# Kernel tuning notes

Hardware: AMD Instinct MI355X
Metric: run time of the kernel (lower is better)

Reference implementation:

```python
import jax, jax.numpy as jnp
import numpy as np

B, N, H, T = 4096, 512, 1024, 10  # batch, input_size, hidden_size, num_iterations
NUM_OPS = 20


def setup_inputs() -> dict:
    key = jax.random.key(0)
    k1, k2, k3, k4 = jax.random.split(key, 4)
    return {
        "x": jax.random.normal(k1, (B, N, 1), jnp.float32),
        "frozen_weight": jax.random.normal(k2, (1, N, H), jnp.float32) / np.sqrt(H),
        "alpha": jax.random.normal(k3, (T, NUM_OPS), jnp.float32),
        "layer_beta": jax.random.normal(k4, (T, 2), jnp.float32),
    }


def _softshrink(x, lam):
    return jnp.where(x > lam, x - lam, jnp.where(x < -lam, x + lam, jnp.zeros_like(x)))


def _hardshrink(x, lam):
    return jnp.where(jnp.abs(x) > lam, x, jnp.zeros_like(x))


def _make_ops(lam):
    # Same 20 ops, same order as the torch ModuleList.
    return [
        lambda x: _softshrink(x, lam),                 # Softshrink(0.001/L)
        jax.nn.relu,                                   # ReLU
        lambda x: x,                                   # Identity
        lambda x: jax.nn.gelu(x, approximate=False),   # GELU (exact erf, torch default)
        jax.nn.elu,                                    # ELU
        lambda x: _hardshrink(x, lam),                 # Hardshrink(0.001/L)
        lambda x: jnp.clip(x, -1.0, 1.0),              # Hardtanh
        jax.nn.hard_swish,                             # Hardswish
        jax.nn.selu,                                   # SELU
        jax.nn.celu,                                   # CELU
        jax.nn.leaky_relu,                             # LeakyReLU (slope 0.01)
        jax.nn.log_sigmoid,                            # LogSigmoid
        lambda x: x - jnp.tanh(x),                     # Tanhshrink
        jax.nn.soft_sign,                              # Softsign
        jax.nn.softplus,                               # Softplus
        jnp.tanh,                                      # Tanh
        jax.nn.sigmoid,                                # Sigmoid
        jax.nn.hard_sigmoid,                           # Hardsigmoid
        jax.nn.silu,                                   # SiLU
        lambda x: x * jnp.tanh(jax.nn.softplus(x)),    # Mish
    ]


def _forward(x, frozen_weight, alpha, layer_beta):
    W = frozen_weight[0]                       # [N, H]
    L = jnp.linalg.norm(W, ord=2) ** 2         # spectral norm squared (Lipschitz)
    lam = 0.001 / L
    ops = _make_ops(lam)

    b = x.shape[0]
    hidden = W.shape[1]
    z = jnp.zeros((b, hidden, 1), dtype=x.dtype)
    z_prev = z
    num_iters = alpha.shape[0]
    for i in range(num_iters):
        aw = jax.nn.softmax(alpha[i])          # [20] (training path, eval_flag=False)
        bw = jax.nn.softmax(layer_beta[i])     # [2]
        # FISTA-style momentum + frozen-weight gradient step
        z_aux = z + (i / (i + 3)) * (z - z_prev)      # [B,H,1]
        Wz = jnp.einsum('nh,bho->bno', W, z_aux)      # [B,N,1]
        grad = jnp.einsum('nh,bno->bho', W, Wz - x)   # [B,H,1]
        z_g = z_aux - grad / L
        # 20-way weighted activation mixture
        z_op = aw[0] * ops[0](z_g)
        for w, op in zip(aw[1:], ops[1:]):
            z_op = z_op + w * op(z_g)
        # beta-weighted residual mix becomes z_prev; z_op becomes current_z
        z_prev = z * bw[0] + z_op * bw[1]
        z = z_op
    return z


def reference(x, frozen_weight, alpha, layer_beta):
    return _forward(x, frozen_weight, alpha, layer_beta)
```

## Files before the change

kernel.cpp:

```cpp
#include <hip/hip_runtime.h>
#include <hip/hip_bf16.h>

#define DI __device__ __forceinline__

typedef float f32x4 __attribute__((ext_vector_type(4)));
typedef __bf16 bf16x8 __attribute__((ext_vector_type(8)));
using bf16_t = __hip_bfloat16;
using ushort_t = unsigned short;

DI void gload_lds16(const void* g, void* l) {
  __builtin_amdgcn_global_load_lds(
      (const __attribute__((address_space(1))) void*)g,
      (__attribute__((address_space(3))) void*)l, 16, 0, 0);
}

DI float rcpf(float x) { return __builtin_amdgcn_rcpf(x); }

DI float act_mix(float x, const float* aw, float lam) {
  const float ax  = fabsf(x);
  const float en  = __expf(-ax);
  const float en2 = en * en;
  const float i1  = rcpf(1.0f + en);
  const float sig = (x >= 0.0f) ? i1 : en * i1;
  const float th  = copysignf((1.0f - en2) * rcpf(1.0f + en2), x);
  const float l1p = __logf(1.0f + en);
  const float sp  = fmaxf(x, 0.0f) + l1p;
  const float lsg = fminf(x, 0.0f) - l1p;
  const float q   = ((x >= 0.0f) ? en2 : 1.0f) * (i1 * i1);
  const float mish = x * (1.0f - q) * rcpf(1.0f + q);
  const float u  = 0.7071067811865476f * x;
  const float au = fabsf(u);
  const float t  = rcpf(1.0f + 0.3275911f * au);
  float poly = fmaf(t, 1.061405429f, -1.453152027f);
  poly = fmaf(t, poly, 1.421413741f);
  poly = fmaf(t, poly, -0.284496736f);
  poly = fmaf(t, poly, 0.254829592f);
  poly *= t;
  const float erfa = 1.0f - poly * __expf(-u * u);
  const float gelu = 0.5f * x * (1.0f + copysignf(erfa, x));
  const float em1  = en - 1.0f;
  const float elu  = (x > 0.0f) ? x : em1;
  const float selu = (x > 0.0f) ? 1.0507009873554805f * x : 1.7580993408473766f * em1;
  const float relu = fmaxf(x, 0.0f);
  const float t6   = fminf(fmaxf(x + 3.0f, 0.0f), 6.0f) * 0.16666666666666666f;
  const float ssh  = (x > lam) ? (x - lam) : ((x < -lam) ? (x + lam) : 0.0f);
  const float hsh  = (ax > lam) ? x : 0.0f;
  const float htan = fminf(fmaxf(x, -1.0f), 1.0f);
  const float lky  = (x >= 0.0f) ? x : 0.01f * x;
  const float ssn  = x * rcpf(1.0f + ax);
  float r = aw[0] * ssh;
  r = fmaf(aw[1],  relu,   r);
  r = fmaf(aw[2],  x,      r);
  r = fmaf(aw[3],  gelu,   r);
  r = fmaf(aw[4],  elu,    r);
  r = fmaf(aw[5],  hsh,    r);
  r = fmaf(aw[6],  htan,   r);
  r = fmaf(aw[7],  x * t6, r);
  r = fmaf(aw[8],  selu,   r);
  r = fmaf(aw[9],  elu,    r);
  r = fmaf(aw[10], lky,    r);
  r = fmaf(aw[11], lsg,    r);
  r = fmaf(aw[12], x - th, r);
  r = fmaf(aw[13], ssn,    r);
  r = fmaf(aw[14], sp,     r);
  r = fmaf(aw[15], th,     r);
  r = fmaf(aw[16], sig,    r);
  r = fmaf(aw[17], t6,     r);
  r = fmaf(aw[18], x * sig, r);
  r = fmaf(aw[19], mish,   r);
  return r;
}

__global__ void k_prep(const float* __restrict__ W, const float* __restrict__ x,
                       bf16_t* __restrict__ Whi, bf16_t* __restrict__ Wlo,
                       bf16_t* __restrict__ Wth, bf16_t* __restrict__ Wtl,
                       bf16_t* __restrict__ xh, bf16_t* __restrict__ xl) {
  int i = blockIdx.x * 256 + threadIdx.x;
  if (i < 512 * 1024) {
    float w = W[i];
    bf16_t h = __float2bfloat16(w);
    bf16_t l = __float2bfloat16(w - __bfloat162float(h));
    Whi[i] = h; Wlo[i] = l;
    int n = i >> 10, hc = i & 1023;
    Wth[hc * 512 + n] = h; Wtl[hc * 512 + n] = l;
  }
  int j = i - 512 * 1024;
  if (j >= 0 && j < 4096 * 512) {
    float v = x[j];
    bf16_t h = __float2bfloat16(v);
    xh[j] = h;
    xl[j] = __float2bfloat16(v - __bfloat162float(h));
  }
}

template <int KDIM, bool FIRST, bool WF32>
__global__ __launch_bounds__(256) void k_sqm(
    const bf16_t* __restrict__ Xhi, const bf16_t* __restrict__ Xlo,
    bf16_t* __restrict__ Chi, bf16_t* __restrict__ Clo,
    float* __restrict__ Cf,
    const float* __restrict__ pin, float* __restrict__ pout) {
  __shared__ __align__(16) ushort_t Ah[2][32 * 64], Al[2][32 * 64],
                                    Bh[2][32 * 64], Bl[2][32 * 64];
  __shared__ float red[4];
  const int tid = threadIdx.x, lane = tid & 63, wave = tid >> 6;
  const int wm = wave >> 1, wn = wave & 1;
  const int i0 = blockIdx.x * 32, j0 = blockIdx.y * 32;
  const int bid = blockIdx.y * gridDim.x + blockIdx.x;
  const int r16 = lane & 15, kg = lane >> 4;

  float s = 1.0f;
  if constexpr (!FIRST) {
    float v = pin[tid];
    for (int off = 32; off; off >>= 1) v += __shfl_down(v, off, 64);
    if ((tid & 63) == 0) red[tid >> 6] = v;
    __syncthreads();
    s = 1.0f / (red[0] + red[1] + red[2] + red[3]);
    __syncthreads();
  }

  const int row = tid >> 3;
  const int srcc = (((tid & 7) ^ (row & 7)) << 3);
  const long abase = (long)(i0 + row) * KDIM + srcc;
  const long bbase = (long)(j0 + row) * KDIM + srcc;
  const int ldst = tid * 8;

  auto stage = [&](int buf, int kt) {
    gload_lds16(Xhi + abase + kt, &Ah[buf][ldst]);
    gload_lds16(Xlo + abase + kt, &Al[buf][ldst]);
    gload_lds16(Xhi + bbase + kt, &Bh[buf][ldst]);
    gload_lds16(Xlo + bbase + kt, &Bl[buf][ldst]);
  };

  f32x4 acc = {};
  constexpr int NT = KDIM / 64;
  stage(0, 0);
  __syncthreads();
  for (int t = 0; t < NT; ++t) {
    if (t + 1 < NT) stage((t + 1) & 1, (t + 1) * 64);
    const int b = t & 1;
    const int ra = wm * 16 + r16, rb = wn * 16 + r16;
#pragma unroll
    for (int kk = 0; kk < 64; kk += 32) {
      int oa = ra * 64 + ((kk + kg * 8) ^ ((ra & 7) * 8));
      int ob = rb * 64 + ((kk + kg * 8) ^ ((rb & 7) * 8));
      bf16x8 ah = *(const bf16x8*)&Ah[b][oa];
      bf16x8 al = *(const bf16x8*)&Al[b][oa];
      bf16x8 bh = *(const bf16x8*)&Bh[b][ob];
      bf16x8 bl = *(const bf16x8*)&Bl[b][ob];
      acc = __builtin_amdgcn_mfma_f32_16x16x32_bf16(ah, bh, acc, 0, 0, 0);
      acc = __builtin_amdgcn_mfma_f32_16x16x32_bf16(ah, bl, acc, 0, 0, 0);
      acc = __builtin_amdgcn_mfma_f32_16x16x32_bf16(al, bh, acc, 0, 0, 0);
    }
    __syncthreads();
  }

  float fro = 0.0f;
#pragma unroll
  for (int r = 0; r < 4; ++r) {
    float c = acc[r] * s;
    int orow = i0 + wm * 16 + (lane >> 4) * 4 + r;
    int ocol = j0 + wn * 16 + r16;
    int idx = orow * 512 + ocol;
    bf16_t h = __float2bfloat16(c);
    Chi[idx] = h;
    Clo[idx] = __float2bfloat16(c - __bfloat162float(h));
    if constexpr (WF32) Cf[idx] = c;
    fro = fmaf(c, c, fro);
  }
  for (int off = 32; off; off >>= 1) fro += __shfl_down(fro, off, 64);
  if ((tid & 63) == 0) red[tid >> 6] = fro;
  __syncthreads();
  if (tid == 0) pout[bid] = red[0] + red[1] + red[2] + red[3];
}

__global__ __launch_bounds__(256) void k_G(const bf16_t* __restrict__ Xhi,
                                           const bf16_t* __restrict__ Xlo,
                                           bf16_t* __restrict__ G) {
  __shared__ __align__(16) ushort_t Ah[2][32 * 64], Al[2][32 * 64],
                                    Bh[2][32 * 64], Bl[2][32 * 64];
  const int tid = threadIdx.x, lane = tid & 63, wave = tid >> 6;
  const int wm = wave >> 1, wn = wave & 1;
  const int i0 = blockIdx.x * 32, j0 = blockIdx.y * 32;
  const int r16 = lane & 15, kg = lane >> 4;
  const int row = tid >> 3;
  const int srcc = (((tid & 7) ^ (row & 7)) << 3);
  const long abase = (long)(i0 + row) * 512 + srcc;
  const long bbase = (long)(j0 + row) * 512 + srcc;
  const int ldst = tid * 8;

  auto stage = [&](int buf, int kt) {
    gload_lds16(Xhi + abase + kt, &Ah[buf][ldst]);
    gload_lds16(Xlo + abase + kt, &Al[buf][ldst]);
    gload_lds16(Xhi + bbase + kt, &Bh[buf][ldst]);
    gload_lds16(Xlo + bbase + kt, &Bl[buf][ldst]);
  };

  f32x4 acc = {};
  stage(0, 0);
  __syncthreads();
  for (int t = 0; t < 8; ++t) {
    if (t + 1 < 8) stage((t + 1) & 1, (t + 1) * 64);
    const int b = t & 1;
    const int ra = wm * 16 + r16, rb = wn * 16 + r16;
#pragma unroll
    for (int kk = 0; kk < 64; kk += 32) {
      int oa = ra * 64 + ((kk + kg * 8) ^ ((ra & 7) * 8));
      int ob = rb * 64 + ((kk + kg * 8) ^ ((rb & 7) * 8));
      bf16x8 ah = *(const bf16x8*)&Ah[b][oa];
      bf16x8 al = *(const bf16x8*)&Al[b][oa];
      bf16x8 bh = *(const bf16x8*)&Bh[b][ob];
      bf16x8 bl = *(const bf16x8*)&Bl[b][ob];
      acc = __builtin_amdgcn_mfma_f32_16x16x32_bf16(ah, bh, acc, 0, 0, 0);
      acc = __builtin_amdgcn_mfma_f32_16x16x32_bf16(ah, bl, acc, 0, 0, 0);
      acc = __builtin_amdgcn_mfma_f32_16x16x32_bf16(al, bh, acc, 0, 0, 0);
    }
    __syncthreads();
  }
#pragma unroll
  for (int r = 0; r < 4; ++r) {
    int orow = i0 + wm * 16 + (lane >> 4) * 4 + r;
    int ocol = j0 + wn * 16 + r16;
    G[orow * 1024 + ocol] = __float2bfloat16(acc[r]);
  }
}

__global__ __launch_bounds__(256) void k_xw(const bf16_t* __restrict__ xh_,
                                            const bf16_t* __restrict__ xl_,
                                            const bf16_t* __restrict__ Bh_,
                                            const bf16_t* __restrict__ Bl_,
                                            const float* __restrict__ prm,
                                            bf16_t* __restrict__ out) {
  __shared__ __align__(16) ushort_t Axh[2][64 * 64], Axl[2][64 * 64],
                                    Bwh[2][64 * 64], Bwl[2][64 * 64];
  const int tid = threadIdx.x, lane = tid & 63, wave = tid >> 6;
  const int wm = wave >> 1, wn = wave & 1;
  const int m0 = blockIdx.x * 64, n0 = blockIdx.y * 64;
  const int r16 = lane & 15, kg = lane >> 4;

  auto stage = [&](int buf, int kt) {
#pragma unroll
    for (int q = 0; q < 2; ++q) {
      int lin = (tid + q * 256) * 8;
      int row = lin >> 6;
      int col = ((((lin >> 3) & 7) ^ (row & 7)) << 3);
      gload_lds16(xh_ + (long)(m0 + row) * 512 + kt + col, &Axh[buf][lin]);
      gload_lds16(xl_ + (long)(m0 + row) * 512 + kt + col, &Axl[buf][lin]);
      gload_lds16(Bh_ + (long)(n0 + row) * 512 + kt + col, &Bwh[buf][lin]);
      gload_lds16(Bl_ + (long)(n0 + row) * 512 + kt + col, &Bwl[buf][lin]);
    }
  };

  f32x4 acc[2][2] = {};
  stage(0, 0);
  __syncthreads();
  for (int t = 0; t < 8; ++t) {
    if (t + 1 < 8) stage((t + 1) & 1, (t + 1) * 64);
    const int b = t & 1;
#pragma unroll
    for (int kk = 0; kk < 64; kk += 32) {
      bf16x8 ah[2], al[2], bh[2], bl[2];
#pragma unroll
      for (int f = 0; f < 2; ++f) {
        int ra = wm * 32 + f * 16 + r16;
        int rb = wn * 32 + f * 16 + r16;
        int oa = ra * 64 + ((kk + kg * 8) ^ ((ra & 7) * 8));
        int ob = rb * 64 + ((kk + kg * 8) ^ ((rb & 7) * 8));
        ah[f] = *(const bf16x8*)&Axh[b][oa];
        al[f] = *(const bf16x8*)&Axl[b][oa];
        bh[f] = *(const bf16x8*)&Bwh[b][ob];
        bl[f] = *(const bf16x8*)&Bwl[b][ob];
      }
#pragma unroll
      for (int i = 0; i < 2; ++i)
#pragma unroll
        for (int j = 0; j < 2; ++j) {
          acc[i][j] = __builtin_amdgcn_mfma_f32_16x16x32_bf16(ah[i], bh[j], acc[i][j], 0, 0, 0);
          acc[i][j] = __builtin_amdgcn_mfma_f32_16x16x32_bf16(ah[i], bl[j], acc[i][j], 0, 0, 0);
          acc[i][j] = __builtin_amdgcn_mfma_f32_16x16x32_bf16(al[i], bh[j], acc[i][j], 0, 0, 0);
        }
    }
    __syncthreads();
  }
  const float invL = prm[21];
#pragma unroll
  for (int i = 0; i < 2; ++i)
#pragma unroll
    for (int j = 0; j < 2; ++j)
#pragma unroll
      for (int r = 0; r < 4; ++r) {
        int row = m0 + wm * 32 + i * 16 + (lane >> 4) * 4 + r;
        int col = n0 + wn * 32 + j * 16 + r16;
        out[(long)row * 1024 + col] = __float2bfloat16(acc[i][j][r] * invL);
      }
}

__global__ __launch_bounds__(256) void k_dot(const float* __restrict__ A0,
                                             const float* __restrict__ B,
                                             float* __restrict__ numP,
                                             float* __restrict__ denP) {
  __shared__ float redn[4], redd[4];
  const int tid = threadIdx.x;
  const int idx4 = blockIdx.x * 256 + tid;
  const f32x4 a = ((const f32x4*)A0)[idx4];
  const f32x4 b = ((const f32x4*)B)[idx4];
  float nv = a[0]*b[0] + a[1]*b[1] + a[2]*b[2] + a[3]*b[3];
  float dv = 0.0f;
#pragma unroll
  for (int q = 0; q < 4; ++q) {
    int i = idx4 * 4 + q;
    if ((i >> 9) == (i & 511)) dv += b[q];
  }
  for (int off = 32; off; off >>= 1) {
    nv += __shfl_down(nv, off, 64);
    dv += __shfl_down(dv, off, 64);
  }
  if ((tid & 63) == 0) { redn[tid >> 6] = nv; redd[tid >> 6] = dv; }
  __syncthreads();
  if (tid == 0) {
    numP[blockIdx.x] = redn[0] + redn[1] + redn[2] + redn[3];
    denP[blockIdx.x] = redd[0] + redd[1] + redd[2] + redd[3];
  }
}

__global__ __launch_bounds__(256) void k_setup(const float* __restrict__ alpha,
                                               const float* __restrict__ beta,
                                               const float* __restrict__ numP,
                                               const float* __restrict__ denP,
                                               float* __restrict__ params) {
  __shared__ float redn[4], redd[4];
  __shared__ float Lsh;
  const int tid = threadIdx.x;
  float nv = numP[tid], dv = denP[tid];
  for (int off = 32; off; off >>= 1) {
    nv += __shfl_down(nv, off, 64);
    dv += __shfl_down(dv, off, 64);
  }
  if ((tid & 63) == 0) { redn[tid >> 6] = nv; redd[tid >> 6] = dv; }
  __syncthreads();
  if (tid == 0)
    Lsh = (redn[0] + redn[1] + redn[2] + redn[3]) /
          (redd[0] + redd[1] + redd[2] + redd[3]);
  __syncthreads();
  const int t = tid;
  if (t >= 10) return;
  float L = Lsh;
  float invL = 1.0f / L;
  float lam = 0.001f * invL;
  const float* a = alpha + t * 20;
  float mx = a[0];
  for (int k = 1; k < 20; ++k) mx = fmaxf(mx, a[k]);
  float e[20], ssum = 0.0f;
  for (int k = 0; k < 20; ++k) { e[k] = expf(a[k] - mx); ssum += e[k]; }
  float inv = 1.0f / ssum;
  float* P = params + t * 32;
  for (int k = 0; k < 20; ++k) P[k] = e[k] * inv;
  float b0 = beta[t * 2], b1 = beta[t * 2 + 1];
  float bm = fmaxf(b0, b1);
  float eb0 = expf(b0 - bm), eb1 = expf(b1 - bm);
  float bw0 = eb0 / (eb0 + eb1);
  P[20] = ((float)(t + 1) / (float)(t + 4)) * bw0;
  P[21] = invL;
  P[22] = lam;
  P[23] = L;
}

__global__ __launch_bounds__(256) void k_it0(const bf16_t* __restrict__ xWs,
                                             bf16_t* __restrict__ zauxN,
                                             bf16_t* __restrict__ zB,
                                             const float* __restrict__ prm) {
  const long i = ((long)blockIdx.x * 256 + threadIdx.x) * 8;
  const float d = prm[20], lam = prm[22];
  float aw[20];
#pragma unroll
  for (int k = 0; k < 20; ++k) aw[k] = prm[k];
  bf16x8 v = *(const bf16x8*)(const void*)(xWs + i);
#pragma unroll
  for (int r = 0; r < 8; ++r) {
    float zop = act_mix((float)v[r], aw, lam);
    zB[i + r] = __float2bfloat16(zop);
    zauxN[i + r] = __float2bfloat16(zop * (1.0f + d));
  }
}

template <bool LAST>
__global__ __launch_bounds__(256, 4) void k_iter(const bf16_t* __restrict__ A,
                                                 const bf16_t* __restrict__ G,
                                                 const bf16_t* __restrict__ xWs,
                                                 bf16_t* __restrict__ zauxN,
                                                 bf16_t* zB, float* zio,
                                                 const float* __restrict__ prm) {
  __shared__ __align__(16) ushort_t As[2][64 * 64], Bs[2][64 * 64];
  const int tid = threadIdx.x, lane = tid & 63, wave = tid >> 6;
  const int wm = wave >> 1, wn = wave & 1;
  const int bid = blockIdx.x;
  const int swz = (bid & 7) * 128 + (bid >> 3);
  const int m0 = (swz >> 4) * 64, n0 = (swz & 15) * 64;
  const int r16 = lane & 15, kg = lane >> 4;

  auto stage = [&](int buf, int kt) {
#pragma unroll
    for (int q = 0; q < 2; ++q) {
      int lin = (tid + q * 256) * 8;
      int row = lin >> 6;
      int col = ((((lin >> 3) & 7) ^ (row & 7)) << 3);
      gload_lds16(A + (long)(m0 + row) * 1024 + kt + col, &As[buf][lin]);
      gload_lds16(G + (long)(n0 + row) * 1024 + kt + col, &Bs[buf][lin]);
    }
  };

  f32x4 acc[2][2] = {};
  auto compute = [&](int b) {
#pragma unroll
    for (int kk = 0; kk < 64; kk += 32) {
      bf16x8 a[2], bb[2];
#pragma unroll
      for (int f = 0; f < 2; ++f) {
        int ra = wm * 32 + f * 16 + r16;
        int rb = wn * 32 + f * 16 + r16;
        a[f]  = *(const bf16x8*)&As[b][ra * 64 + ((kk + kg * 8) ^ ((ra & 7) * 8))];
        bb[f] = *(const bf16x8*)&Bs[b][rb * 64 + ((kk + kg * 8) ^ ((rb & 7) * 8))];
      }
#pragma unroll
      for (int i = 0; i < 2; ++i)
#pragma unroll
        for (int j = 0; j < 2; ++j)
          acc[i][j] = __builtin_amdgcn_mfma_f32_16x16x32_bf16(a[i], bb[j], acc[i][j], 0, 0, 0);
    }
  };

  stage(0, 0);
  stage(1, 64);
  asm volatile("s_waitcnt vmcnt(4)" ::: "memory");
  __builtin_amdgcn_s_barrier();
  __builtin_amdgcn_sched_barrier(0);

  for (int t = 0; t < 16; ++t) {
    compute(t & 1);
    if (t == 15) break;
    asm volatile("s_waitcnt lgkmcnt(0)" ::: "memory");
    __builtin_amdgcn_sched_barrier(0);
    __builtin_amdgcn_s_barrier();
    if (t + 2 < 16) {
      stage(t & 1, (t + 2) * 64);
      asm volatile("s_waitcnt vmcnt(4)" ::: "memory");
    } else {
      asm volatile("s_waitcnt vmcnt(0)" ::: "memory");
    }
    __builtin_amdgcn_s_barrier();
    __builtin_amdgcn_sched_barrier(0);
  }
  __builtin_amdgcn_sched_barrier(0);

  const float d_i = prm[20];
  const float invL = prm[21];
  const float lam = prm[22];
  float aw[20];
#pragma unroll
  for (int k = 0; k < 20; ++k) aw[k] = prm[k];

  float xv[2][2][4], av[2][2][4], zv[2][2][4];
#pragma unroll
  for (int i = 0; i < 2; ++i)
#pragma unroll
    for (int j = 0; j < 2; ++j)
#pragma unroll
      for (int r = 0; r < 4; ++r) {
        int row = m0 + wm * 32 + i * 16 + (lane >> 4) * 4 + r;
        int col = n0 + wn * 32 + j * 16 + r16;
        long idx = (long)row * 1024 + col;
        xv[i][j][r] = __bfloat162float(xWs[idx]);
        av[i][j][r] = __bfloat162float(A[idx]);
        if (!LAST) zv[i][j][r] = __bfloat162float(zB[idx]);
      }
#pragma unroll
  for (int i = 0; i < 2; ++i)
#pragma unroll
    for (int j = 0; j < 2; ++j)
#pragma unroll
      for (int r = 0; r < 4; ++r) {
        int row = m0 + wm * 32 + i * 16 + (lane >> 4) * 4 + r;
        int col = n0 + wn * 32 + j * 16 + r16;
        long idx = (long)row * 1024 + col;
        float zg = fmaf(-acc[i][j][r], invL, av[i][j][r] + xv[i][j][r]);
        float zop = act_mix(zg, aw, lam);
        if (LAST) {
          zio[idx] = zop;
        } else {
          zB[idx] = __float2bfloat16(zop);
          zauxN[idx] = __float2bfloat16(fmaf(d_i, zop - zv[i][j][r], zop));
        }
      }
}

extern "C" void kernel_launch(void* const* d_in, const int* in_sizes, int n_in,
                              void* d_out, int out_size, void* d_ws, size_t ws_size,
                              hipStream_t stream) {
  const float* x     = (const float*)d_in[0];
  const float* W     = (const float*)d_in[1];
  const float* alpha = (const float*)d_in[2];
  const float* beta  = (const float*)d_in[3];
  float* zout = (float*)d_out;

  char* ws = (char*)d_ws;
  const size_t MB = 1u << 20;
  float* pb[11];
  for (int k = 0; k < 11; ++k) pb[k] = (float*)(ws + (size_t)k * 1024);
  float* numP   = (float*)(ws + 12 * 1024);
  float* denP   = (float*)(ws + 13 * 1024);
  float* params = (float*)(ws + 14 * 1024);
  const size_t HDR = 32768;
  float*  A0f  = (float*)(ws + HDR);
  float*  Bf   = (float*)(ws + HDR + 1 * MB);
  bf16_t* H0   = (bf16_t*)(ws + HDR + 2 * MB);
  bf16_t* L0   = (bf16_t*)(ws + HDR + 2 * MB + 512 * 1024);
  bf16_t* H1   = (bf16_t*)(ws + HDR + 3 * MB);
  bf16_t* L1   = (bf16_t*)(ws + HDR + 3 * MB + 512 * 1024);
  bf16_t* Whi  = (bf16_t*)(ws + HDR + 4 * MB);
  bf16_t* Wlo  = (bf16_t*)(ws + HDR + 5 * MB);
  bf16_t* Wth  = (bf16_t*)(ws + HDR + 6 * MB);
  bf16_t* Wtl  = (bf16_t*)(ws + HDR + 7 * MB);
  bf16_t* Gm   = (bf16_t*)(ws + HDR + 8 * MB);
  bf16_t* xh   = (bf16_t*)(ws + HDR + 10 * MB);
  bf16_t* xl   = (bf16_t*)(ws + HDR + 14 * MB);
  bf16_t* xWs  = (bf16_t*)(ws + HDR + 18 * MB);
  bf16_t* zx0  = (bf16_t*)(ws + HDR + 26 * MB);
  bf16_t* zx1  = (bf16_t*)(ws + HDR + 34 * MB);
  bf16_t* zB   = (bf16_t*)(ws + HDR + 42 * MB);

  k_prep<<<10240, 256, 0, stream>>>(W, x, Whi, Wlo, Wth, Wtl, xh, xl);

  k_sqm<1024, true, true><<<dim3(16, 16), 256, 0, stream>>>(
      Whi, Wlo, H0, L0, A0f, nullptr, pb[0]);
  bf16_t* Hs[2] = {H0, H1};
  bf16_t* Ls[2] = {L0, L1};
  int pp = 0;
  for (int k = 0; k < 9; ++k) {
    if (k == 8)
      k_sqm<512, false, true><<<dim3(16, 16), 256, 0, stream>>>(
          Hs[pp], Ls[pp], Hs[pp ^ 1], Ls[pp ^ 1], Bf, pb[k], pb[k + 1]);
    else
      k_sqm<512, false, false><<<dim3(16, 16), 256, 0, stream>>>(
          Hs[pp], Ls[pp], Hs[pp ^ 1], Ls[pp ^ 1], nullptr, pb[k], pb[k + 1]);
    pp ^= 1;
  }
  k_dot<<<256, 256, 0, stream>>>(A0f, Bf, numP, denP);
  k_setup<<<1, 256, 0, stream>>>(alpha, beta, numP, denP, params);

  k_G<<<dim3(32, 32), 256, 0, stream>>>(Wth, Wtl, Gm);
  k_xw<<<dim3(64, 16), 256, 0, stream>>>(xh, xl, Wth, Wtl, params, xWs);

  k_it0<<<2048, 256, 0, stream>>>(xWs, zx1, zB, params);

  bf16_t* zx[2] = {zx0, zx1};
  for (int i = 1; i < 9; ++i)
    k_iter<false><<<1024, 256, 0, stream>>>(zx[i & 1], Gm, xWs, zx[(i + 1) & 1],
                                            zB, zout, params + i * 32);
  k_iter<true><<<1024, 256, 0, stream>>>(zx[9 & 1], Gm, xWs, zx0 ,
                                         zB, zout, params + 9 * 32);
}
```

Before: 381.1 us.

## Fuse iteration-0 activation into xW epilogue and triple-buffer iter GEMM loads

Removes the separate k_it0 kernel by computing the activation mixture, zB and the first z_aux directly in the k_xw epilogue. This saves one launch and a full re-read of xWs. Separately, k_iter moves from double to triple LDS buffering with a deeper prefetch and adjusted vmcnt waits, trading occupancy (launch bound 4 to 3) for more load latency hiding. The waitcnt bookkeeping for the tail iterations must be exact for correctness.

```diff
diff --git a/kernel.cpp b/kernel.cpp
--- a/kernel.cpp
+++ b/kernel.cpp
@@ -229,7 +229,9 @@
                                             const bf16_t* __restrict__ Bh_,
                                             const bf16_t* __restrict__ Bl_,
                                             const float* __restrict__ prm,
-                                            bf16_t* __restrict__ out) {
+                                            bf16_t* __restrict__ out,
+                                            bf16_t* __restrict__ zB,
+                                            bf16_t* __restrict__ zaux1) {
   __shared__ __align__(16) ushort_t Axh[2][64 * 64], Axl[2][64 * 64],
                                     Bwh[2][64 * 64], Bwl[2][64 * 64];
   const int tid = threadIdx.x, lane = tid & 63, wave = tid >> 6;
@@ -282,6 +284,11 @@
     __syncthreads();
   }
   const float invL = prm[21];
+  const float d0 = prm[20];
+  const float lam = prm[22];
+  float aw[20];
+#pragma unroll
+  for (int k = 0; k < 20; ++k) aw[k] = prm[k];
 #pragma unroll
   for (int i = 0; i < 2; ++i)
 #pragma unroll
@@ -290,7 +297,12 @@
       for (int r = 0; r < 4; ++r) {
         int row = m0 + wm * 32 + i * 16 + (lane >> 4) * 4 + r;
         int col = n0 + wn * 32 + j * 16 + r16;
-        out[(long)row * 1024 + col] = __float2bfloat16(acc[i][j][r] * invL);
+        long idx = (long)row * 1024 + col;
+        bf16_t xb = __float2bfloat16(acc[i][j][r] * invL);
+        out[idx] = xb;
+        float zop = act_mix(__bfloat162float(xb), aw, lam);
+        zB[idx] = __float2bfloat16(zop);
+        zaux1[idx] = __float2bfloat16(zop * (1.0f + d0));
       }
 }
 
@@ -364,32 +376,14 @@
   P[23] = L;
 }
 
-__global__ __launch_bounds__(256) void k_it0(const bf16_t* __restrict__ xWs,
-                                             bf16_t* __restrict__ zauxN,
-                                             bf16_t* __restrict__ zB,
-                                             const float* __restrict__ prm) {
-  const long i = ((long)blockIdx.x * 256 + threadIdx.x) * 8;
-  const float d = prm[20], lam = prm[22];
-  float aw[20];
-#pragma unroll
-  for (int k = 0; k < 20; ++k) aw[k] = prm[k];
-  bf16x8 v = *(const bf16x8*)(const void*)(xWs + i);
-#pragma unroll
-  for (int r = 0; r < 8; ++r) {
-    float zop = act_mix((float)v[r], aw, lam);
-    zB[i + r] = __float2bfloat16(zop);
-    zauxN[i + r] = __float2bfloat16(zop * (1.0f + d));
-  }
-}
-
 template <bool LAST>
-__global__ __launch_bounds__(256, 4) void k_iter(const bf16_t* __restrict__ A,
+__global__ __launch_bounds__(256, 3) void k_iter(const bf16_t* __restrict__ A,
                                                  const bf16_t* __restrict__ G,
                                                  const bf16_t* __restrict__ xWs,
                                                  bf16_t* __restrict__ zauxN,
                                                  bf16_t* zB, float* zio,
                                                  const float* __restrict__ prm) {
-  __shared__ __align__(16) ushort_t As[2][64 * 64], Bs[2][64 * 64];
+  __shared__ __align__(16) ushort_t As[3][64 * 64], Bs[3][64 * 64];
   const int tid = threadIdx.x, lane = tid & 63, wave = tid >> 6;
   const int wm = wave >> 1, wn = wave & 1;
   const int bid = blockIdx.x;
@@ -430,18 +424,21 @@
 
   stage(0, 0);
   stage(1, 64);
-  asm volatile("s_waitcnt vmcnt(4)" ::: "memory");
+  stage(2, 128);
+  asm volatile("s_waitcnt vmcnt(8)" ::: "memory");
   __builtin_amdgcn_s_barrier();
   __builtin_amdgcn_sched_barrier(0);
 
   for (int t = 0; t < 16; ++t) {
-    compute(t & 1);
+    compute(t % 3);
     if (t == 15) break;
     asm volatile("s_waitcnt lgkmcnt(0)" ::: "memory");
     __builtin_amdgcn_sched_barrier(0);
     __builtin_amdgcn_s_barrier();
-    if (t + 2 < 16) {
-      stage(t & 1, (t + 2) * 64);
+    if (t + 3 < 16) {
+      stage(t % 3, (t + 3) * 64);
+      asm volatile("s_waitcnt vmcnt(8)" ::: "memory");
+    } else if (t == 13) {
       asm volatile("s_waitcnt vmcnt(4)" ::: "memory");
     } else {
       asm volatile("s_waitcnt vmcnt(0)" ::: "memory");
@@ -547,9 +544,7 @@
   k_setup<<<1, 256, 0, stream>>>(alpha, beta, numP, denP, params);
 
   k_G<<<dim3(32, 32), 256, 0, stream>>>(Wth, Wtl, Gm);
-  k_xw<<<dim3(64, 16), 256, 0, stream>>>(xh, xl, Wth, Wtl, params, xWs);
-
-  k_it0<<<2048, 256, 0, stream>>>(xWs, zx1, zB, params);
+  k_xw<<<dim3(64, 16), 256, 0, stream>>>(xh, xl, Wth, Wtl, params, xWs, zB, zx1);
 
   bf16_t* zx[2] = {zx0, zx1};
   for (int i = 1; i < 9; ++i)
```

Measured after the change: 405.5 us (median of 2 runs). 1.06x slower.
